# Performance work log

Hardware: AMD Instinct MI355X
Metric: run time of the kernel (lower is better)

Reference implementation:

```python
import jax, jax.numpy as jnp
from jax import lax
import numpy as np

ALPHA = 2.0
EROSIONS = 10


def setup_inputs() -> dict:
    key = jax.random.key(0)
    k1, k2 = jax.random.split(key)
    b, c, h, w = 32, 1, 1024, 1024
    pred = jax.random.uniform(k1, (b, c, h, w), dtype=jnp.float32)
    target = jax.random.randint(k2, (b, c, h, w), 0, 2, dtype=jnp.int32)
    return {"pred": pred, "target": target}


def _perform_erosion(bound, kernel, alpha, erosions):
    # bound: (b, 1, H, W); kernel: (1, 1, 3, 3) cross * 0.2
    def step(carry, k):
        bnd, eroted = carry
        dilation = lax.conv_general_dilated(bnd, kernel, window_strides=(1, 1), padding="SAME")
        erosion = jnp.maximum(dilation - 0.5, 0.0)
        # per-sample global max/min over channel+spatial dims
        emax = jnp.max(erosion, axis=(1, 2, 3), keepdims=True)
        emin = jnp.min(erosion, axis=(1, 2, 3), keepdims=True)
        denom = emax - emin
        safe = jnp.where(denom != 0, denom, jnp.ones_like(denom))
        erosion = jnp.where(denom != 0, (erosion - emin) / safe, erosion)
        eroted = eroted + erosion * (k + 1.0) ** alpha
        return (erosion, eroted), None

    init = (bound, jnp.zeros_like(bound))
    (_, eroted), _ = lax.scan(step, init, jnp.arange(erosions, dtype=bound.dtype))
    return eroted


def reference(pred, target):
    # cross-shaped 3x3 erosion kernel scaled by 0.2 (fixed buffer)
    cross = jnp.array([[0.0, 1.0, 0.0], [1.0, 1.0, 1.0], [0.0, 1.0, 0.0]], dtype=pred.dtype) * 0.2
    kernel = cross[None, None]  # (1, 1, 3, 3)
    c = pred.shape[1]
    losses = []
    for i in range(c):
        tgt = (target == i).astype(pred.dtype)  # (b, c, H, W); c==1 here
        bound = (pred[:, i : i + 1] - tgt) ** 2
        eroted = _perform_erosion(bound, kernel, ALPHA, EROSIONS)
        losses.append(jnp.mean(eroted))
    return jnp.mean(jnp.stack(losses))
```

## Files before the change

kernel.cpp:

```cpp
#include <hip/hip_runtime.h>
#include <hip/hip_fp16.h>

#define BATCH 32
#define H 1024
#define W 1024
#define NPIX (H * W)
#define ITERS 10
#define SROWS 16
#define BROWS 32
#define STRIPS (H / BROWS)

typedef _Float16 half8_t __attribute__((ext_vector_type(8)));

struct Stats {
    unsigned maxbits[ITERS][BATCH];
    unsigned minbits[ITERS][BATCH];
    double   sum[ITERS][BATCH];
};

__global__ void init_stats(Stats* st) {
    int i = blockIdx.x * blockDim.x + threadIdx.x;
    if (i < ITERS * BATCH) {
        (&st->maxbits[0][0])[i] = 0u;
        (&st->minbits[0][0])[i] = 0x7f800000u;
        (&st->sum[0][0])[i]     = 0.0;
    }
}

__device__ __forceinline__ float bound1(const float* __restrict__ pred,
                                        const int* __restrict__ tgt, size_t off) {
    float d = pred[off] - (tgt[off] == 0 ? 1.f : 0.f);
    return d * d;
}

template <int MODE>
__device__ __forceinline__ void row_load8(
    const float* __restrict__ pred, const int* __restrict__ target,
    const _Float16* __restrict__ in, size_t base, int r, int lane128,
    float sent, float f[8], float& L, float& R)
{
    const int  col = lane128 * 8;
    const bool inb = (r >= 0) && (r < H);
    size_t off = base + (size_t)r * W + col;
    if (inb) {
        if (MODE == 0) {
            float4 p0 = *(const float4*)(pred + off);
            float4 p1 = *(const float4*)(pred + off + 4);
            int4   t0 = *(const int4*)(target + off);
            int4   t1 = *(const int4*)(target + off + 4);
            float d;
            d = p0.x - (t0.x == 0 ? 1.f : 0.f); f[0] = d * d;
            d = p0.y - (t0.y == 0 ? 1.f : 0.f); f[1] = d * d;
            d = p0.z - (t0.z == 0 ? 1.f : 0.f); f[2] = d * d;
            d = p0.w - (t0.w == 0 ? 1.f : 0.f); f[3] = d * d;
            d = p1.x - (t1.x == 0 ? 1.f : 0.f); f[4] = d * d;
            d = p1.y - (t1.y == 0 ? 1.f : 0.f); f[5] = d * d;
            d = p1.z - (t1.z == 0 ? 1.f : 0.f); f[6] = d * d;
            d = p1.w - (t1.w == 0 ? 1.f : 0.f); f[7] = d * d;
        } else {
            half8_t x = *(const half8_t*)(in + off);
            #pragma unroll
            for (int j = 0; j < 8; ++j)
                f[j] = (float)x[j];
        }
    } else {
        #pragma unroll
        for (int j = 0; j < 8; ++j) f[j] = sent;
    }

    L = __shfl_up(f[7], 1, 64);
    R = __shfl_down(f[0], 1, 64);

    const int wl = lane128 & 63;
    if (!inb) { L = sent; R = sent; return; }
    if (lane128 == 0) {
        L = sent;
    } else if (wl == 0) {
        size_t o = off - 1;
        L = (MODE == 0) ? bound1(pred, target, o) : (float)in[o];
    }
    if (lane128 == 127) {
        R = sent;
    } else if (wl == 63) {
        size_t o = off + 8;
        R = (MODE == 0) ? bound1(pred, target, o) : (float)in[o];
    }
}

template <int MODE, int STORE>
__global__ __launch_bounds__(256) void erode_strip(
    const float* __restrict__ pred, const int* __restrict__ target,
    const _Float16* __restrict__ in, _Float16* __restrict__ out,
    Stats* __restrict__ st, int iter)
{
    const int blk = blockIdx.x;
    const int b   = blk >> 5;
    const int s   = blk & (STRIPS - 1);
    const int tid = threadIdx.x;
    const int sub     = tid >> 7;
    const int lane128 = tid & 127;
    const int r0  = s * BROWS + sub * SROWS;
    const int col = lane128 * 8;
    const size_t base = (size_t)b * NPIX;

    float sent = 0.f, A = 0.2f, Bc = -0.5f;
    if (MODE == 1) {
        float emax = __uint_as_float(st->maxbits[iter - 1][b]);
        float emn  = __uint_as_float(st->minbits[iter - 1][b]);
        float denom = emax - emn;
        if (denom != 0.f) {
            float invd = 1.f / denom;
            sent = emn;
            A    = 0.2f * invd;
            Bc   = -emn * invd - 0.5f;
        }
    }

    float prev[8], cur[8], nxt[8];
    float Lp, Rp, Lc, Rc, Ln, Rn;
    row_load8<MODE>(pred, target, in, base, r0 - 1, lane128, sent, prev, Lp, Rp);
    row_load8<MODE>(pred, target, in, base, r0,     lane128, sent, cur,  Lc, Rc);

    float  m  = 0.f;
    float  mn = __builtin_inf();
    double sum = 0.0;

    #pragma unroll 2
    for (int i = 0; i < SROWS; ++i) {
        const int r = r0 + i;
        row_load8<MODE>(pred, target, in, base, r + 1, lane128, sent, nxt, Ln, Rn);

        float e[8];
        #pragma unroll
        for (int j = 0; j < 8; ++j) {
            float lf = (j == 0) ? Lc : cur[j - 1];
            float rf = (j == 7) ? Rc : cur[j + 1];
            float s5 = (cur[j] + lf) + (rf + prev[j]) + nxt[j];
            e[j] = fmaxf(fmaf(s5, A, Bc), 0.f);
        }

        if (STORE) {
            half8_t o;
            #pragma unroll
            for (int j = 0; j < 8; ++j) o[j] = (_Float16)e[j];
            *(half8_t*)(out + base + (size_t)r * W + col) = o;
        }

        float rm = fmaxf(fmaxf(fmaxf(e[0], e[1]), fmaxf(e[2], e[3])),
                         fmaxf(fmaxf(e[4], e[5]), fmaxf(e[6], e[7])));
        float rn = fminf(fminf(fminf(e[0], e[1]), fminf(e[2], e[3])),
                         fminf(fminf(e[4], e[5]), fminf(e[6], e[7])));
        float rs = ((e[0] + e[1]) + (e[2] + e[3])) + ((e[4] + e[5]) + (e[6] + e[7]));
        m   = fmaxf(m, rm);
        mn  = fminf(mn, rn);
        sum += (double)rs;

        #pragma unroll
        for (int j = 0; j < 8; ++j) { prev[j] = cur[j]; cur[j] = nxt[j]; }
        Lc = Ln; Rc = Rn;
    }

    #pragma unroll
    for (int off = 32; off > 0; off >>= 1) {
        m   = fmaxf(m,  __shfl_down(m,  off, 64));
        mn  = fminf(mn, __shfl_down(mn, off, 64));
        sum += __shfl_down(sum, off, 64);
    }
    __shared__ float  smax[4];
    __shared__ float  smin[4];
    __shared__ double ssum[4];
    int lane = tid & 63, wave = tid >> 6;
    if (lane == 0) { smax[wave] = m; smin[wave] = mn; ssum[wave] = sum; }
    __syncthreads();
    if (tid == 0) {
        m   = fmaxf(fmaxf(smax[0], smax[1]), fmaxf(smax[2], smax[3]));
        mn  = fminf(fminf(smin[0], smin[1]), fminf(smin[2], smin[3]));
        sum = ssum[0] + ssum[1] + ssum[2] + ssum[3];
        atomicMax(&st->maxbits[iter][b], __float_as_uint(m));
        atomicMin(&st->minbits[iter][b], __float_as_uint(mn));
        atomicAdd(&st->sum[iter][b], sum);
    }
}

__global__ void finalize(const Stats* __restrict__ st, float* __restrict__ out) {
    if (threadIdx.x == 0 && blockIdx.x == 0) {
        double total = 0.0;
        for (int k = 0; k < ITERS; ++k) {
            double w = (double)((k + 1) * (k + 1));
            for (int b = 0; b < BATCH; ++b) {
                float emax  = __uint_as_float(st->maxbits[k][b]);
                float emn   = __uint_as_float(st->minbits[k][b]);
                float denom = emax - emn;
                double s = st->sum[k][b];
                double sn;
                if (denom != 0.f)
                    sn = (s - (double)NPIX * (double)emn) / (double)denom;
                else
                    sn = s;
                total += w * sn;
            }
        }
        out[0] = (float)(total / ((double)BATCH * (double)NPIX));
    }
}

extern "C" void kernel_launch(void* const* d_in, const int* in_sizes, int n_in,
                              void* d_out, int out_size, void* d_ws, size_t ws_size,
                              hipStream_t stream) {
    (void)in_sizes; (void)n_in; (void)out_size;
    const float* pred   = (const float*)d_in[0];
    const int*   target = (const int*)d_in[1];

    const size_t fieldBytes = (size_t)BATCH * NPIX * sizeof(_Float16);
    char* ws = (char*)d_ws;
    _Float16* bufA;
    _Float16* bufB;
    Stats* st;
    if (ws_size >= 2 * fieldBytes + sizeof(Stats)) {
        bufA = (_Float16*)ws;
        bufB = (_Float16*)(ws + fieldBytes);
        st   = (Stats*)(ws + 2 * fieldBytes);
    } else {
        bufA = (_Float16*)ws;
        bufB = (_Float16*)d_in[1];
        st   = (Stats*)(ws + fieldBytes);
    }

    init_stats<<<1, 320, 0, stream>>>(st);

    dim3 grid(BATCH * STRIPS), block(256);
    erode_strip<0, 1><<<grid, block, 0, stream>>>(pred, target, nullptr, bufA, st, 0);

    _Float16* src = bufA;
    _Float16* dst = bufB;
    for (int k = 1; k < ITERS; ++k) {
        if (k == ITERS - 1)
            erode_strip<1, 0><<<grid, block, 0, stream>>>(nullptr, nullptr, src, dst, st, k);
        else
            erode_strip<1, 1><<<grid, block, 0, stream>>>(nullptr, nullptr, src, dst, st, k);
        _Float16* t = src; src = dst; dst = t;
    }

    finalize<<<1, 64, 0, stream>>>(st, (float*)d_out);
}
```

Measured before the change: 577.4 us.

## Fuse all erosion iterations into one cooperative kernel with register-resident strips

Replaces the ten per-iteration kernel launches with a single cooperative-groups kernel. Each block keeps its 32-row strip in registers as fp16 across all iterations and exchanges only boundary rows through small global halo buffers, with a grid.sync between iterations. This removes the full-field read and write through HBM on every iteration and the launch gaps between kernels. In exchange it requires all 1024 blocks to be co-resident, adds grid-wide barrier costs and register pressure, and keeps the old multi-launch path as a fallback.

Result: no change. 586.1 us (+1.5%).

```diff
diff --git a/kernel.cpp b/kernel.cpp
--- a/kernel.cpp
+++ b/kernel.cpp
@@ -1,5 +1,8 @@
 #include <hip/hip_runtime.h>
 #include <hip/hip_fp16.h>
+#include <hip/hip_cooperative_groups.h>
+
+namespace cg = cooperative_groups;
 
 #define BATCH 32
 #define H 1024
@@ -9,6 +12,7 @@
 #define SROWS 16
 #define BROWS 32
 #define STRIPS (H / BROWS)
+#define NBLK (BATCH * STRIPS)
 
 typedef _Float16 half8_t __attribute__((ext_vector_type(8)));
 
@@ -31,6 +35,251 @@
                                         const int* __restrict__ tgt, size_t off) {
     float d = pred[off] - (tgt[off] == 0 ? 1.f : 0.f);
     return d * d;
+}
+
+__device__ __forceinline__ void cvt8(half8_t x, float f[8]) {
+    #pragma unroll
+    for (int j = 0; j < 8; ++j) f[j] = (float)x[j];
+}
+
+__device__ __forceinline__ void row_load0(
+    const float* __restrict__ pred, const int* __restrict__ target,
+    size_t base, int r, int lane128, float f[8], float& L, float& R)
+{
+    const int  col = lane128 * 8;
+    const bool inb = (r >= 0) && (r < H);
+    size_t off = base + (size_t)r * W + col;
+    if (inb) {
+        float4 p0 = *(const float4*)(pred + off);
+        float4 p1 = *(const float4*)(pred + off + 4);
+        int4   t0 = *(const int4*)(target + off);
+        int4   t1 = *(const int4*)(target + off + 4);
+        float d;
+        d = p0.x - (t0.x == 0 ? 1.f : 0.f); f[0] = d * d;
+        d = p0.y - (t0.y == 0 ? 1.f : 0.f); f[1] = d * d;
+        d = p0.z - (t0.z == 0 ? 1.f : 0.f); f[2] = d * d;
+        d = p0.w - (t0.w == 0 ? 1.f : 0.f); f[3] = d * d;
+        d = p1.x - (t1.x == 0 ? 1.f : 0.f); f[4] = d * d;
+        d = p1.y - (t1.y == 0 ? 1.f : 0.f); f[5] = d * d;
+        d = p1.z - (t1.z == 0 ? 1.f : 0.f); f[6] = d * d;
+        d = p1.w - (t1.w == 0 ? 1.f : 0.f); f[7] = d * d;
+    } else {
+        #pragma unroll
+        for (int j = 0; j < 8; ++j) f[j] = 0.f;
+    }
+    L = __shfl_up(f[7], 1, 64);
+    R = __shfl_down(f[0], 1, 64);
+    const int wl = lane128 & 63;
+    if (!inb) { L = 0.f; R = 0.f; return; }
+    if (lane128 == 0)        L = 0.f;
+    else if (wl == 0)        L = bound1(pred, target, off - 1);
+    if (lane128 == 127)      R = 0.f;
+    else if (wl == 63)       R = bound1(pred, target, off + 8);
+}
+
+__global__ __launch_bounds__(256, 4) void erode_fused(
+    const float* __restrict__ pred, const int* __restrict__ target,
+    _Float16* __restrict__ haloTop,
+    _Float16* __restrict__ haloBot,
+    Stats* __restrict__ st)
+{
+    cg::grid_group grid = cg::this_grid();
+    const int blk = blockIdx.x;
+    const int b   = blk >> 5;
+    const int s   = blk & (STRIPS - 1);
+    const int tid = threadIdx.x;
+    const int sub     = tid >> 7;
+    const int lane128 = tid & 127;
+    const int wv      = tid >> 6;
+    const int lane    = tid & 63;
+    const int r0  = s * BROWS + sub * SROWS;
+    const int col = lane128 * 8;
+    const size_t base = (size_t)b * NPIX;
+
+    __shared__ _Float16 eL[4][SROWS];
+    __shared__ _Float16 eR[4][SROWS];
+    __shared__ half8_t  rowA[128];
+    __shared__ half8_t  rowB[128];
+    __shared__ float  smax[4];
+    __shared__ float  smin[4];
+    __shared__ double ssum[4];
+
+    half8_t stor[SROWS];
+
+    {
+        float prev[8], cur[8], nxt[8];
+        float Lp, Rp, Lc, Rc, Ln, Rn;
+        row_load0(pred, target, base, r0 - 1, lane128, prev, Lp, Rp);
+        row_load0(pred, target, base, r0,     lane128, cur,  Lc, Rc);
+
+        float  m  = 0.f;
+        float  mn = __builtin_inf();
+        double sum = 0.0;
+
+        #pragma unroll
+        for (int i = 0; i < SROWS; ++i) {
+            row_load0(pred, target, base, r0 + i + 1, lane128, nxt, Ln, Rn);
+            float e[8];
+            #pragma unroll
+            for (int j = 0; j < 8; ++j) {
+                float lf = (j == 0) ? Lc : cur[j - 1];
+                float rf = (j == 7) ? Rc : cur[j + 1];
+                float s5 = (cur[j] + lf) + (rf + prev[j]) + nxt[j];
+                e[j] = fmaxf(fmaf(s5, 0.2f, -0.5f), 0.f);
+            }
+            half8_t o;
+            #pragma unroll
+            for (int j = 0; j < 8; ++j) o[j] = (_Float16)e[j];
+            stor[i] = o;
+
+            float rm = fmaxf(fmaxf(fmaxf(e[0], e[1]), fmaxf(e[2], e[3])),
+                             fmaxf(fmaxf(e[4], e[5]), fmaxf(e[6], e[7])));
+            float rn = fminf(fminf(fminf(e[0], e[1]), fminf(e[2], e[3])),
+                             fminf(fminf(e[4], e[5]), fminf(e[6], e[7])));
+            float rs = ((e[0] + e[1]) + (e[2] + e[3])) + ((e[4] + e[5]) + (e[6] + e[7]));
+            m   = fmaxf(m, rm);
+            mn  = fminf(mn, rn);
+            sum += (double)rs;
+            #pragma unroll
+            for (int j = 0; j < 8; ++j) { prev[j] = cur[j]; cur[j] = nxt[j]; }
+            Lc = Ln; Rc = Rn;
+        }
+
+        #pragma unroll
+        for (int off = 32; off > 0; off >>= 1) {
+            m   = fmaxf(m,  __shfl_down(m,  off, 64));
+            mn  = fminf(mn, __shfl_down(mn, off, 64));
+            sum += __shfl_down(sum, off, 64);
+        }
+        if (lane == 0) { smax[wv] = m; smin[wv] = mn; ssum[wv] = sum; }
+        __syncthreads();
+        if (tid == 0) {
+            m   = fmaxf(fmaxf(smax[0], smax[1]), fmaxf(smax[2], smax[3]));
+            mn  = fminf(fminf(smin[0], smin[1]), fminf(smin[2], smin[3]));
+            sum = ssum[0] + ssum[1] + ssum[2] + ssum[3];
+            atomicMax(&st->maxbits[0][b], __float_as_uint(m));
+            atomicMin(&st->minbits[0][b], __float_as_uint(mn));
+            atomicAdd(&st->sum[0][b], sum);
+        }
+        if (sub == 0) *(half8_t*)(haloTop + ((size_t)1 * NBLK + blk) * W + col) = stor[0];
+        else          *(half8_t*)(haloBot + ((size_t)1 * NBLK + blk) * W + col) = stor[SROWS - 1];
+    }
+    grid.sync();
+
+    for (int k = 1; k < ITERS; ++k) {
+        const int par = k & 1;
+
+        unsigned mb = __hip_atomic_load(&st->maxbits[k - 1][b], __ATOMIC_RELAXED, __HIP_MEMORY_SCOPE_AGENT);
+        unsigned nb = __hip_atomic_load(&st->minbits[k - 1][b], __ATOMIC_RELAXED, __HIP_MEMORY_SCOPE_AGENT);
+        float emax = __uint_as_float(mb);
+        float emn  = __uint_as_float(nb);
+        float denom = emax - emn;
+        float sent = 0.f, A = 0.2f, Bc = -0.5f;
+        if (denom != 0.f) {
+            float invd = 1.f / denom;
+            sent = emn;
+            A    = 0.2f * invd;
+            Bc   = -emn * invd - 0.5f;
+        }
+
+        #pragma unroll
+        for (int i = 0; i < SROWS; ++i) {
+            if (lane == 0)  eL[wv][i] = stor[i][0];
+            if (lane == 63) eR[wv][i] = stor[i][7];
+        }
+        if (sub == 0) rowA[lane128] = stor[SROWS - 1];
+        else          rowB[lane128] = stor[0];
+        __syncthreads();
+
+        float fprev[8], fcur[8], fnxt[8];
+        if (sub == 0) {
+            if (s > 0) {
+                half8_t h = *(const half8_t*)(haloBot + ((size_t)par * NBLK + blk - 1) * W + col);
+                cvt8(h, fprev);
+            } else {
+                #pragma unroll
+                for (int j = 0; j < 8; ++j) fprev[j] = sent;
+            }
+        } else {
+            cvt8(rowA[lane128], fprev);
+        }
+        cvt8(stor[0], fcur);
+        half8_t hdn = {};
+        if (sub == 1 && s < STRIPS - 1)
+            hdn = *(const half8_t*)(haloTop + ((size_t)par * NBLK + blk + 1) * W + col);
+
+        float  m  = 0.f;
+        float  mn = __builtin_inf();
+        double sum = 0.0;
+
+        #pragma unroll
+        for (int i = 0; i < SROWS; ++i) {
+            if (i < SROWS - 1)       cvt8(stor[i + 1], fnxt);
+            else if (sub == 0)       cvt8(rowB[lane128], fnxt);
+            else if (s < STRIPS - 1) cvt8(hdn, fnxt);
+            else {
+                #pragma unroll
+                for (int j = 0; j < 8; ++j) fnxt[j] = sent;
+            }
+
+            float L = __shfl_up(fcur[7], 1, 64);
+            float R = __shfl_down(fcur[0], 1, 64);
+            if (lane128 == 0)        L = sent;
+            else if (lane == 0)      L = (float)eR[wv - 1][i];
+            if (lane128 == 127)      R = sent;
+            else if (lane == 63)     R = (float)eL[wv + 1][i];
+
+            float e[8];
+            #pragma unroll
+            for (int j = 0; j < 8; ++j) {
+                float lf = (j == 0) ? L : fcur[j - 1];
+                float rf = (j == 7) ? R : fcur[j + 1];
+                float s5 = (fcur[j] + lf) + (rf + fprev[j]) + fnxt[j];
+                e[j] = fmaxf(fmaf(s5, A, Bc), 0.f);
+            }
+
+            half8_t o;
+            #pragma unroll
+            for (int j = 0; j < 8; ++j) o[j] = (_Float16)e[j];
+            stor[i] = o;
+
+            float rm = fmaxf(fmaxf(fmaxf(e[0], e[1]), fmaxf(e[2], e[3])),
+                             fmaxf(fmaxf(e[4], e[5]), fmaxf(e[6], e[7])));
+            float rn = fminf(fminf(fminf(e[0], e[1]), fminf(e[2], e[3])),
+                             fminf(fminf(e[4], e[5]), fminf(e[6], e[7])));
+            float rs = ((e[0] + e[1]) + (e[2] + e[3])) + ((e[4] + e[5]) + (e[6] + e[7]));
+            m   = fmaxf(m, rm);
+            mn  = fminf(mn, rn);
+            sum += (double)rs;
+
+            #pragma unroll
+            for (int j = 0; j < 8; ++j) { fprev[j] = fcur[j]; fcur[j] = fnxt[j]; }
+        }
+
+        #pragma unroll
+        for (int off = 32; off > 0; off >>= 1) {
+            m   = fmaxf(m,  __shfl_down(m,  off, 64));
+            mn  = fminf(mn, __shfl_down(mn, off, 64));
+            sum += __shfl_down(sum, off, 64);
+        }
+        if (lane == 0) { smax[wv] = m; smin[wv] = mn; ssum[wv] = sum; }
+        __syncthreads();
+        if (tid == 0) {
+            m   = fmaxf(fmaxf(smax[0], smax[1]), fmaxf(smax[2], smax[3]));
+            mn  = fminf(fminf(smin[0], smin[1]), fminf(smin[2], smin[3]));
+            sum = ssum[0] + ssum[1] + ssum[2] + ssum[3];
+            atomicMax(&st->maxbits[k][b], __float_as_uint(m));
+            atomicMin(&st->minbits[k][b], __float_as_uint(mn));
+            atomicAdd(&st->sum[k][b], sum);
+        }
+
+        if (k < ITERS - 1) {
+            const int np = (k + 1) & 1;
+            if (sub == 0) *(half8_t*)(haloTop + ((size_t)np * NBLK + blk) * W + col) = stor[0];
+            else          *(half8_t*)(haloBot + ((size_t)np * NBLK + blk) * W + col) = stor[SROWS - 1];
+            grid.sync();
+        }
+    }
 }
 
 template <int MODE>
@@ -60,31 +309,20 @@
         } else {
             half8_t x = *(const half8_t*)(in + off);
             #pragma unroll
-            for (int j = 0; j < 8; ++j)
-                f[j] = (float)x[j];
+            for (int j = 0; j < 8; ++j) f[j] = (float)x[j];
         }
     } else {
         #pragma unroll
         for (int j = 0; j < 8; ++j) f[j] = sent;
     }
-
     L = __shfl_up(f[7], 1, 64);
     R = __shfl_down(f[0], 1, 64);
-
     const int wl = lane128 & 63;
     if (!inb) { L = sent; R = sent; return; }
-    if (lane128 == 0) {
-        L = sent;
-    } else if (wl == 0) {
-        size_t o = off - 1;
-        L = (MODE == 0) ? bound1(pred, target, o) : (float)in[o];
-    }
-    if (lane128 == 127) {
-        R = sent;
-    } else if (wl == 63) {
-        size_t o = off + 8;
-        R = (MODE == 0) ? bound1(pred, target, o) : (float)in[o];
-    }
+    if (lane128 == 0)        L = sent;
+    else if (wl == 0)        L = (MODE == 0) ? bound1(pred, target, off - 1) : (float)in[off - 1];
+    if (lane128 == 127)      R = sent;
+    else if (wl == 63)       R = (MODE == 0) ? bound1(pred, target, off + 8) : (float)in[off + 8];
 }
 
 template <int MODE, int STORE>
@@ -129,7 +367,6 @@
     for (int i = 0; i < SROWS; ++i) {
         const int r = r0 + i;
         row_load8<MODE>(pred, target, in, base, r + 1, lane128, sent, nxt, Ln, Rn);
-
         float e[8];
         #pragma unroll
         for (int j = 0; j < 8; ++j) {
@@ -138,14 +375,12 @@
             float s5 = (cur[j] + lf) + (rf + prev[j]) + nxt[j];
             e[j] = fmaxf(fmaf(s5, A, Bc), 0.f);
         }
-
         if (STORE) {
             half8_t o;
             #pragma unroll
             for (int j = 0; j < 8; ++j) o[j] = (_Float16)e[j];
             *(half8_t*)(out + base + (size_t)r * W + col) = o;
         }
-
         float rm = fmaxf(fmaxf(fmaxf(e[0], e[1]), fmaxf(e[2], e[3])),
                          fmaxf(fmaxf(e[4], e[5]), fmaxf(e[6], e[7])));
         float rn = fminf(fminf(fminf(e[0], e[1]), fminf(e[2], e[3])),
@@ -154,7 +389,6 @@
         m   = fmaxf(m, rm);
         mn  = fminf(mn, rn);
         sum += (double)rs;
-
         #pragma unroll
         for (int j = 0; j < 8; ++j) { prev[j] = cur[j]; cur[j] = nxt[j]; }
         Lc = Ln; Rc = Rn;
@@ -225,20 +459,43 @@
         bufB = (_Float16*)d_in[1];
         st   = (Stats*)(ws + fieldBytes);
     }
+    _Float16* haloT = (_Float16*)ws;
+    _Float16* haloB = haloT + (size_t)2 * NBLK * W;
+
+    static int mode = -1;
+    if (mode < 0) {
+        int coop = 0;
+        (void)hipDeviceGetAttribute(&coop, hipDeviceAttributeCooperativeLaunch, 0);
+        int perCU = 0;
+        (void)hipOccupancyMaxActiveBlocksPerMultiprocessor(&perCU, erode_fused, 256, 0);
+        int nCU = 0;
+        (void)hipDeviceGetAttribute(&nCU, hipDeviceAttributeMultiprocessorCount, 0);
+        mode = (coop && perCU > 0 && nCU > 0 && (long)perCU * nCU >= NBLK) ? 1 : 0;
+    }
 
     init_stats<<<1, 320, 0, stream>>>(st);
 
-    dim3 grid(BATCH * STRIPS), block(256);
-    erode_strip<0, 1><<<grid, block, 0, stream>>>(pred, target, nullptr, bufA, st, 0);
-
-    _Float16* src = bufA;
-    _Float16* dst = bufB;
-    for (int k = 1; k < ITERS; ++k) {
-        if (k == ITERS - 1)
-            erode_strip<1, 0><<<grid, block, 0, stream>>>(nullptr, nullptr, src, dst, st, k);
-        else
-            erode_strip<1, 1><<<grid, block, 0, stream>>>(nullptr, nullptr, src, dst, st, k);
-        _Float16* t = src; src = dst; dst = t;
+    bool ran_fused = false;
+    if (mode == 1) {
+        void* args[5] = { (void*)&pred, (void*)&target, (void*)&haloT, (void*)&haloB, (void*)&st };
+        hipError_t e = hipLaunchCooperativeKernel((void*)erode_fused, dim3(NBLK), dim3(256),
+                                                  args, 0, stream);
+        if (e == hipSuccess) ran_fused = true;
+        else mode = 0;
+    }
+
+    if (!ran_fused) {
+        dim3 grid(NBLK), block(256);
+        erode_strip<0, 1><<<grid, block, 0, stream>>>(pred, target, nullptr, bufA, st, 0);
+        _Float16* src = bufA;
+        _Float16* dst = bufB;
+        for (int k = 1; k < ITERS; ++k) {
+            if (k == ITERS - 1)
+                erode_strip<1, 0><<<grid, block, 0, stream>>>(nullptr, nullptr, src, dst, st, k);
+            else
+                erode_strip<1, 1><<<grid, block, 0, stream>>>(nullptr, nullptr, src, dst, st, k);
+            _Float16* t = src; src = dst; dst = t;
+        }
     }
 
     finalize<<<1, 64, 0, stream>>>(st, (float*)d_out);
```
